# Optimization experiments

Hardware: AMD Instinct MI355X
Metric: run time of the kernel (lower is better)

Reference implementation:

```python
import jax, jax.numpy as jnp
import numpy as np
import math


def _forward(x, f0, theta, sigma, theta0, fbs, mix, w1, b1, w2, b2, conv_w):
    B, I, H, W = x.shape          # config requires B == I == H (== W here)
    S, O, _ = f0.shape            # config requires O == 1
    # ---- log-Gabor filter bank, fully vectorized over (scale, out, in) ----
    yy = jnp.linspace(-1.0, 1.0, H)[:, None]   # meshgrid 'ij': y along rows
    xx = jnp.linspace(-1.0, 1.0, W)[None, :]
    r = jnp.sqrt(xx ** 2 + yy ** 2 + 1e-6)     # [H,W]
    phi = jnp.arctan2(yy, xx)                  # [H,W]
    lr = jnp.log(r)
    log_gabor = jnp.exp(-(lr - jnp.log(f0)[..., None, None]) ** 2
                        / (2.0 * jnp.log(sigma)[..., None, None] ** 2))
    angular = jnp.exp(-(phi - theta[..., None, None]) ** 2
                      / (2.0 * theta0[..., None, None] ** 2))
    filters = log_gabor * angular              # [S,O,I,H,W]
    # ---- FFT (torch fftshift default shifts ALL dims; jnp matches) ----
    xs = jnp.fft.fftshift(jnp.fft.fft2(x))     # [B,I,H,W] complex64
    # ---- frequency attention (two 1x1 convs + softmax over scales) ----
    h1 = jax.nn.relu(jnp.einsum('bchw,oc->bohw', jnp.abs(xs), w1)
                     + b1[None, :, None, None])
    aw = jax.nn.softmax(jnp.einsum('bchw,sc->bshw', h1, w2)
                        + b2[None, :, None, None], axis=1)   # [B,S,H,W]
    # ---- attention-weighted combine. Faithful to torch broadcasting with
    # O==1 and B==I: attended[0,b,i,h,w] = sum_s xs[b,i]*F[s,0,i]*aw[i,s] ----
    attended = jnp.einsum('bihw,sihw,ishw->bihw', xs, filters[:, 0], aw)[None]
    # ---- dynamic frequency band mask (torch slices dims 2,3 = (Cin,H)) ----
    s_idx = jnp.floor((fbs[0, :, 0] + 1.0) / 2.0 * H).astype(jnp.int32)  # [I]
    e_idx = jnp.floor((fbs[0, :, 1] + 1.0) / 2.0 * H).astype(jnp.int32)
    arI = jnp.arange(I)
    arH = jnp.arange(H)
    mk = (arI[None, :] >= s_idx[:, None]) & (arI[None, :] < e_idx[:, None])  # [J,I]
    mh = (arH[None, :] >= s_idx[:, None]) & (arH[None, :] < e_idx[:, None])  # [J,H]
    mask = (mk[:, :, None] & mh[:, None, :]).astype(x.dtype)                 # [J,I,H]
    attended = attended * mask[None, :, :, :, None]
    # ---- back to spatial domain ----
    x_filtered = jnp.fft.ifft2(jnp.fft.ifftshift(attended)).real  # [1,B,I,H,W]
    # ---- spatial 3x3 conv path ----
    x_spatial = jax.lax.conv_general_dilated(
        x, conv_w, window_strides=(1, 1), padding=((1, 1), (1, 1)),
        dimension_numbers=('NCHW', 'OIHW', 'NCHW'))               # [B,1,H,W]
    return mix * x_filtered + (1.0 - mix) * x_spatial[None]


def setup_inputs() -> dict:
    key = jax.random.key(0)
    ks = jax.random.split(key, 10)
    B = I = H = W = 64
    O, S, HID = 1, 3, 64
    PI = math.pi
    x = jax.random.normal(ks[0], (B, I, H, W), dtype=jnp.float32)
    f0 = jnp.ones((S, O, I), jnp.float32)
    theta0 = jnp.ones((S, O, I), jnp.float32)
    sigma = jax.random.uniform(ks[1], (S, O, I), jnp.float32) * PI
    theta = jax.random.uniform(ks[2], (S, O, I), jnp.float32) * PI
    fbs = jax.random.uniform(ks[3], (O, I, 2), jnp.float32)
    mix = jax.random.uniform(ks[4], (1,), jnp.float32)
    w1 = jax.random.normal(ks[5], (HID, I), jnp.float32) * 0.05
    b1 = jnp.zeros((HID,), jnp.float32)
    w2 = jax.random.normal(ks[6], (S, HID), jnp.float32) * 0.05
    b2 = jnp.zeros((S,), jnp.float32)
    conv_w = jax.random.normal(ks[7], (O, I, 3, 3), jnp.float32) / math.sqrt(I * 9)
    return {'x': x, 'f0': f0, 'theta': theta, 'sigma': sigma, 'theta0': theta0,
            'fbs': fbs, 'mix': mix, 'w1': w1, 'b1': b1, 'w2': w2, 'b2': b2,
            'conv_w': conv_w}


def reference(x, f0, theta, sigma, theta0, fbs, mix, w1, b1, w2, b2, conv_w):
    return _forward(x, f0, theta, sigma, theta0, fbs, mix, w1, b1, w2, b2, conv_w)
```

## Files before the change

### kernel.cpp

```cpp
#include <hip/hip_runtime.h>

#define PI_D 3.14159265358979323846

namespace {
constexpr float CT[33] = {
  1.0000000000f,  0.9951847267f,  0.9807852804f,  0.9569403357f,
  0.9238795325f,  0.8819212643f,  0.8314696123f,  0.7730104534f,
  0.7071067812f,  0.6343932842f,  0.5555702330f,  0.4713967368f,
  0.3826834324f,  0.2902846773f,  0.1950903220f,  0.0980171403f,
  0.0f,          -0.0980171403f, -0.1950903220f, -0.2902846773f,
 -0.3826834324f, -0.4713967368f, -0.5555702330f, -0.6343932842f,
 -0.7071067812f, -0.7730104534f, -0.8314696123f, -0.8819212643f,
 -0.9238795325f, -0.9569403357f, -0.9807852804f, -0.9951847267f,
 -1.0f};
constexpr float STb[33] = {
  0.0f,           0.0980171403f,  0.1950903220f,  0.2902846773f,
  0.3826834324f,  0.4713967368f,  0.5555702330f,  0.6343932842f,
  0.7071067812f,  0.7730104534f,  0.8314696123f,  0.8819212643f,
  0.9238795325f,  0.9569403357f,  0.9807852804f,  0.9951847267f,
  1.0f,           0.9951847267f,  0.9807852804f,  0.9569403357f,
  0.9238795325f,  0.8819212643f,  0.8314696123f,  0.7730104534f,
  0.7071067812f,  0.6343932842f,  0.5555702330f,  0.4713967368f,
  0.3826834324f,  0.2902846773f,  0.1950903220f,  0.0980171403f,
  0.0f};
}

__device__ __forceinline__ void bitrev64(float v[64]) {
#pragma unroll
  for (int i = 0; i < 64; ++i) {
    const int j = (int)(__brev((unsigned)i) >> 26);
    if (j > i) { const float tv = v[i]; v[i] = v[j]; v[j] = tv; }
  }
}

template <bool INV, bool REAL>
__device__ __forceinline__ void fft64_stages(float re[64], float im[64]) {
#pragma unroll
  for (int s = 0; s < 6; ++s) {
    const int half = 1 << s;
    const int m = half << 1;
    const int tstep = 32 >> s;
#pragma unroll
    for (int k = 0; k < 64; k += m) {
#pragma unroll
      for (int j = 0; j < half; ++j) {
        const int ti = j * tstep;
        const int a = k + j, b = k + j + half;
        if (REAL && j == 0) {
          const float tr = re[b];
          re[b] = re[a] - tr;
          re[a] = re[a] + tr;
        } else if (REAL && ti == 16) {
          const float t0 = re[b];
          re[b] = re[a];
          im[b] = t0;
          im[a] = -t0;
        } else {
          float tr, tii;
          if (ti == 0) {
            tr = re[b]; tii = im[b];
          } else if (ti == 16) {
            if (INV) { tr = -im[b]; tii = re[b]; }
            else     { tr =  im[b]; tii = -re[b]; }
          } else {
            const float wr = CT[ti];
            const float wi = INV ? STb[ti] : -STb[ti];
            tr  = re[b] * wr - im[b] * wi;
            tii = re[b] * wi + im[b] * wr;
          }
          re[b] = re[a] - tr;  im[b] = im[a] - tii;
          re[a] = re[a] + tr;  im[a] = im[a] + tii;
        }
      }
    }
  }
}

template <bool INV>
__device__ __forceinline__ void fft64_regs(float re[64], float im[64]) {
  bitrev64(re);
  bitrev64(im);
  fft64_stages<INV, false>(re, im);
}

__device__ __forceinline__ void fft64_fwd_real(float re[64], float im[64]) {
  bitrev64(re);
  fft64_stages<false, true>(re, im);
}

__device__ __forceinline__ void band_from_fbs(const float* __restrict__ fbs,
                                              int c, int& s0, int& e0) {
  s0 = (int)floorf((fbs[2 * c]     + 1.0f) * 0.5f * 64.0f);
  e0 = (int)floorf((fbs[2 * c + 1] + 1.0f) * 0.5f * 64.0f);
}

__global__ __launch_bounds__(64) void k_fft_fwd(const float* __restrict__ x,
                                                float* __restrict__ F,
                                                const float* __restrict__ fbs,
                                                const float* __restrict__ w1,
                                                float* __restrict__ w1T) {
  __shared__ float buf[64][65];
  const int t = threadIdx.x;
  const int img = blockIdx.x;
  if (img == 0) {
    for (int k = 0; k < 64; ++k) w1T[t * 64 + k] = w1[k * 64 + t];
  }
  const float* xp = x + ((size_t)img << 12);
  const float4* xr4 = reinterpret_cast<const float4*>(xp + (t << 6));
  float re[64], im[64];
#pragma unroll
  for (int q = 0; q < 16; ++q) {
    const float4 v = xr4[q];
    re[4 * q]     = v.x; re[4 * q + 1] = v.y;
    re[4 * q + 2] = v.z; re[4 * q + 3] = v.w;
  }
#pragma unroll
  for (int j = 0; j < 64; ++j) im[j] = 0.0f;
  fft64_fwd_real(re, im);
#pragma unroll
  for (int j = 0; j < 64; ++j) buf[t][j] = re[j];
  __syncthreads();
#pragma unroll
  for (int j = 0; j < 64; ++j) re[j] = buf[j][t];
  __syncthreads();
#pragma unroll
  for (int j = 0; j < 64; ++j) buf[t][j] = im[j];
  __syncthreads();
#pragma unroll
  for (int j = 0; j < 64; ++j) im[j] = buf[j][t];
  fft64_regs<false>(re, im);
  const int b = img >> 6, i = img & 63;
  const int b_s = (b + 32) & 63, i_s = (i + 32) & 63;
  int s0, e0;
  band_from_fbs(fbs, b_s, s0, e0);
  float* Fre = F + ((size_t)img << 13);
  if ((i_s >= s0) && (i_s < e0)) {
    float* Fim = Fre + 4096;
#pragma unroll
    for (int j = 0; j < 64; ++j) {
      Fre[j * 64 + t] = re[j];
      Fim[j * 64 + t] = im[j];
    }
  } else {
#pragma unroll
    for (int j = 0; j < 64; ++j)
      Fre[j * 64 + t] = sqrtf(re[j] * re[j] + im[j] * im[j]);
  }
}

__global__ __launch_bounds__(256, 4) void k_attn_conv(
    const float* __restrict__ F, const float* __restrict__ w1T,
    const float* __restrict__ b1, const float* __restrict__ w2,
    const float* __restrict__ b2, const float* __restrict__ f0,
    const float* __restrict__ theta, const float* __restrict__ sigma,
    const float* __restrict__ theta0, const float* __restrict__ fbs,
    float* __restrict__ Wc,
    const float* __restrict__ x, const float* __restrict__ cw,
    const float* __restrict__ mixp, float* __restrict__ xsp,
    float* __restrict__ out) {
  __shared__ float part[4][3][64];
  const int t = threadIdx.x;
  const unsigned blk = blockIdx.x;
  const unsigned q5 = blk / 5u;
  const unsigned r5 = blk - q5 * 5u;

  if (r5 == 4u) {
    const int lane = t & 63;
    const int cwv = t >> 6;
    const int b = (int)(q5 >> 4);
    const int row = (int)((q5 & 15u) << 2) | cwv;
    const float* xb = x + ((size_t)b << 18);
    const int rm = row > 0 ? row - 1 : 0;
    const int rp = row < 63 ? row + 1 : 63;
    float P00 = 0.f, P01 = 0.f, P02 = 0.f;
    float P10 = 0.f, P11 = 0.f, P12 = 0.f;
    float P20 = 0.f, P21 = 0.f, P22 = 0.f;
#pragma unroll 4
    for (int ch = 0; ch < 64; ++ch) {
      const float* xc = xb + (ch << 12);
      const float v0 = xc[(rm << 6) + lane];
      const float v1 = xc[(row << 6) + lane];
      const float v2 = xc[(rp << 6) + lane];
      const float* wp = cw + ch * 9;
      P00 = fmaf(v0, wp[0], P00);
      P01 = fmaf(v0, wp[1], P01);
      P02 = fmaf(v0, wp[2], P02);
      P10 = fmaf(v1, wp[3], P10);
      P11 = fmaf(v1, wp[4], P11);
      P12 = fmaf(v1, wp[5], P12);
      P20 = fmaf(v2, wp[6], P20);
      P21 = fmaf(v2, wp[7], P21);
      P22 = fmaf(v2, wp[8], P22);
    }
    const float tmask = (row > 0) ? 1.0f : 0.0f;
    const float bmask = (row < 63) ? 1.0f : 0.0f;
    const float Ql = tmask * P00 + P10 + bmask * P20;
    const float Qm = tmask * P01 + P11 + bmask * P21;
    const float Qr = tmask * P02 + P12 + bmask * P22;
    const float fromL = __shfl_up(Ql, 1, 64);
    const float fromR = __shfl_down(Qr, 1, 64);
    float acc = Qm;
    if (lane > 0) acc += fromL;
    if (lane < 63) acc += fromR;
    xsp[((size_t)b << 12) + (row << 6) + lane] = acc;
    const int b_s = (b + 32) & 63;
    int s0, e0;
    band_from_fbs(fbs, b_s, s0, e0);
    const float val = (1.0f - mixp[0]) * acc;
    float* ob = out + ((size_t)b << 18) + (row << 6) + lane;
#pragma unroll 4
    for (int i2 = 0; i2 < 64; ++i2) {
      const int i_s = (i2 + 32) & 63;
      if (!(i_s >= s0 && i_s < e0)) ob[(size_t)i2 << 12] = val;
    }
    return;
  }

  const int ai = (int)(4u * q5 + r5);
  const int lane = t & 63;
  const int wv = __builtin_amdgcn_readfirstlane(t >> 6);
  const int k0 = wv << 4;
  const int i = ai >> 6;
  const int h = ai & 63;
  const int b_f = (i + 32) & 63;
  const int u_f = (h + 32) & 63;
  const int v_f = (lane + 32) & 63;
  const int pos_f = (u_f << 6) + v_f;
  int s0a, e0a;
  band_from_fbs(fbs, i, s0a, e0a);
  int alo = s0a < 0 ? 0 : (s0a > 64 ? 64 : s0a);
  int ahi = e0a < 0 ? 0 : (e0a > 64 ? 64 : e0a);
  if (ahi < alo) ahi = alo;
  float acc[16];
#pragma unroll
  for (int k = 0; k < 16; ++k) acc[k] = 0.0f;
  const float* Fb = F + ((size_t)(b_f << 6) << 13) + pos_f;
  const float* w1k = w1T + k0;
#pragma unroll 4
  for (int c = 0; c < alo; ++c) {
    const int c_f = (c + 32) & 63;
    const float mc = Fb[(size_t)c_f << 13];
    const float* wrow = w1k + (c << 6);
#pragma unroll
    for (int k = 0; k < 16; ++k) acc[k] = fmaf(wrow[k], mc, acc[k]);
  }
#pragma unroll 2
  for (int c = alo; c < ahi; ++c) {
    const int c_f = (c + 32) & 63;
    const float* base = Fb + ((size_t)c_f << 13);
    const float xr = base[0], xi = base[4096];
    const float mc = sqrtf(xr * xr + xi * xi);
    const float* wrow = w1k + (c << 6);
#pragma unroll
    for (int k = 0; k < 16; ++k) acc[k] = fmaf(wrow[k], mc, acc[k]);
  }
#pragma unroll 4
  for (int c = ahi; c < 64; ++c) {
    const int c_f = (c + 32) & 63;
    const float mc = Fb[(size_t)c_f << 13];
    const float* wrow = w1k + (c << 6);
#pragma unroll
    for (int k = 0; k < 16; ++k) acc[k] = fmaf(wrow[k], mc, acc[k]);
  }
  float p0 = 0.0f, p1 = 0.0f, p2 = 0.0f;
#pragma unroll
  for (int k = 0; k < 16; ++k) {
    const float hv = fmaxf(acc[k] + b1[k0 + k], 0.0f);
    p0 = fmaf(w2[k0 + k], hv, p0);
    p1 = fmaf(w2[64 + k0 + k], hv, p1);
    p2 = fmaf(w2[128 + k0 + k], hv, p2);
  }
  if (wv != 0) {
    part[wv][0][lane] = p0;
    part[wv][1][lane] = p1;
    part[wv][2][lane] = p2;
  }
  __syncthreads();
  if (wv != 0) return;
  float l0 = b2[0] + p0 + part[1][0][lane] + part[2][0][lane] + part[3][0][lane];
  float l1 = b2[1] + p1 + part[1][1][lane] + part[2][1][lane] + part[3][1][lane];
  float l2 = b2[2] + p2 + part[1][2][lane] + part[2][2][lane] + part[3][2][lane];
  float mx = fmaxf(l0, fmaxf(l1, l2));
  float e0v = expf(l0 - mx), e1 = expf(l1 - mx), e2 = expf(l2 - mx);
  float inv = 1.0f / (e0v + e1 + e2);
  float aw0 = e0v * inv, aw1 = e1 * inv, aw2 = e2 * inv;
  const float yy = -1.0f + (float)h * (2.0f / 63.0f);
  const float xx = -1.0f + (float)lane * (2.0f / 63.0f);
  const float r = sqrtf(xx * xx + yy * yy + 1e-6f);
  const float lr = logf(r);
  const float phi = atan2f(yy, xx);
  float wc = 0.0f;
  const float aws[3] = {aw0, aw1, aw2};
#pragma unroll
  for (int s = 0; s < 3; ++s) {
    const float f0v = f0[s * 64 + i];
    const float sgv = sigma[s * 64 + i];
    const float thv = theta[s * 64 + i];
    const float t0v = theta0[s * 64 + i];
    const float ls = logf(sgv);
    const float d1 = lr - logf(f0v);
    const float g1 = expf(-(d1 * d1) / (2.0f * ls * ls));
    const float d2 = phi - thv;
    const float g2 = expf(-(d2 * d2) / (2.0f * t0v * t0v));
    wc = fmaf(g1 * g2, aws[s], wc);
  }
  Wc[((i << 6) + h) * 64 + lane] = wc;
}

__global__ __launch_bounds__(64) void k_ifft_act(
    const float* __restrict__ F, const float* __restrict__ Wc,
    const float* __restrict__ xsp, const float* __restrict__ fbs,
    const float* __restrict__ mixp, float* __restrict__ out) {
  const int img = blockIdx.x;
  const int b = img >> 6, i = img & 63;
  const int b_s = (b + 32) & 63, i_s = (i + 32) & 63;
  int s0, e0;
  band_from_fbs(fbs, b_s, s0, e0);
  if (!((i_s >= s0) && (i_s < e0))) return;
  __shared__ float buf[64][65];
  const int t = threadIdx.x;
  const float* Fre = F + ((size_t)img << 13);
  const float* Fim = Fre + 4096;
  const float* Wcp = Wc + ((size_t)i_s << 12);
  const int u_s = (t + 32) & 63;
  const float rmask = (u_s >= s0 && u_s < e0) ? 1.0f : 0.0f;
  const float* wrow = Wcp + (u_s << 6);
  const float4* fr4 = reinterpret_cast<const float4*>(Fre + (t << 6));
  const float4* fi4 = reinterpret_cast<const float4*>(Fim + (t << 6));
  float re[64], im[64];
#pragma unroll
  for (int q = 0; q < 16; ++q) {
    const int j0 = 4 * q;
    const float4 w4 = *reinterpret_cast<const float4*>(wrow + ((j0 + 32) & 63));
    const float4 vr = fr4[q];
    const float4 vi = fi4[q];
    const float w0 = rmask * w4.x, w1v = rmask * w4.y;
    const float w2v = rmask * w4.z, w3v = rmask * w4.w;
    re[j0]     = vr.x * w0;  re[j0 + 1] = vr.y * w1v;
    re[j0 + 2] = vr.z * w2v; re[j0 + 3] = vr.w * w3v;
    im[j0]     = vi.x * w0;  im[j0 + 1] = vi.y * w1v;
    im[j0 + 2] = vi.z * w2v; im[j0 + 3] = vi.w * w3v;
  }
  fft64_regs<true>(re, im);
#pragma unroll
  for (int j = 0; j < 64; ++j) buf[t][j] = re[j];
  __syncthreads();
#pragma unroll
  for (int j = 0; j < 64; ++j) re[j] = buf[j][t];
  __syncthreads();
#pragma unroll
  for (int j = 0; j < 64; ++j) buf[t][j] = im[j];
  __syncthreads();
#pragma unroll
  for (int j = 0; j < 64; ++j) im[j] = buf[j][t];
  fft64_regs<true>(re, im);
  const float mixv = mixp[0];
  const float sc = mixv * (1.0f / 4096.0f);
  const float om = 1.0f - mixv;
  float* op = out + ((size_t)img << 12);
  const float* xp = xsp + ((size_t)b << 12);
#pragma unroll
  for (int j = 0; j < 64; ++j)
    op[j * 64 + t] = fmaf(sc, re[j], om * xp[j * 64 + t]);
}

extern "C" void kernel_launch(void* const* d_in, const int* in_sizes, int n_in,
                              void* d_out, int out_size, void* d_ws, size_t ws_size,
                              hipStream_t stream) {
  const float* x      = (const float*)d_in[0];
  const float* f0     = (const float*)d_in[1];
  const float* theta  = (const float*)d_in[2];
  const float* sigma  = (const float*)d_in[3];
  const float* theta0 = (const float*)d_in[4];
  const float* fbs    = (const float*)d_in[5];
  const float* mix    = (const float*)d_in[6];
  const float* w1     = (const float*)d_in[7];
  const float* b1     = (const float*)d_in[8];
  const float* w2     = (const float*)d_in[9];
  const float* b2     = (const float*)d_in[10];
  const float* cw     = (const float*)d_in[11];
  float* out = (float*)d_out;
  char* ws = (char*)d_ws;
  float* F   = (float*)(ws);
  float* Wc  = (float*)(ws + 134217728);
  float* xsp = (float*)(ws + 134217728 + 1048576);
  float* w1T = (float*)(ws + 134217728 + 2097152);

  k_fft_fwd<<<4096, 64, 0, stream>>>(x, F, fbs, w1, w1T);
  k_attn_conv<<<5120, 256, 0, stream>>>(F, w1T, b1, w2, b2, f0, theta, sigma,
                                        theta0, fbs, Wc, x, cw, mix, xsp, out);
  k_ifft_act<<<4096, 64, 0, stream>>>(F, Wc, xsp, fbs, mix, out);
}
```

Measured before the change: 212.2 us.

## Split spectrum into dense magnitude buffer and compacted in-band complex buffer

The forward FFT now always writes a dense magnitude array and writes complex spectra only for in-band images, into a compacted buffer indexed by (b<<5)+i. The attention kernel then reads precomputed magnitudes with a uniform, fully unrolled loop that issues 16 loads at a time. This drops the three band-dependent loops and the sqrt-of-complex path from the attention kernel, and halves the stride between its loads. In exchange, in-band images need extra magnitude writes. The compact indexing only avoids collisions and stays inside the buffer if in-band images have i < 32, which holds only when fbs lies in [0,1).

```diff
diff --git a/kernel.cpp b/kernel.cpp
--- a/kernel.cpp
+++ b/kernel.cpp
@@ -95,7 +95,8 @@
 }
 
 __global__ __launch_bounds__(64) void k_fft_fwd(const float* __restrict__ x,
-                                                float* __restrict__ F,
+                                                float* __restrict__ Mag,
+                                                float* __restrict__ Fc,
                                                 const float* __restrict__ fbs,
                                                 const float* __restrict__ w1,
                                                 float* __restrict__ w1T) {
@@ -129,27 +130,27 @@
 #pragma unroll
   for (int j = 0; j < 64; ++j) im[j] = buf[j][t];
   fft64_regs<false>(re, im);
+  float* Mg = Mag + ((size_t)img << 12);
+#pragma unroll
+  for (int j = 0; j < 64; ++j)
+    Mg[j * 64 + t] = sqrtf(re[j] * re[j] + im[j] * im[j]);
   const int b = img >> 6, i = img & 63;
   const int b_s = (b + 32) & 63, i_s = (i + 32) & 63;
   int s0, e0;
   band_from_fbs(fbs, b_s, s0, e0);
-  float* Fre = F + ((size_t)img << 13);
   if ((i_s >= s0) && (i_s < e0)) {
+    float* Fre = Fc + ((size_t)((b << 5) + i) << 13);
     float* Fim = Fre + 4096;
 #pragma unroll
     for (int j = 0; j < 64; ++j) {
       Fre[j * 64 + t] = re[j];
       Fim[j * 64 + t] = im[j];
     }
-  } else {
-#pragma unroll
-    for (int j = 0; j < 64; ++j)
-      Fre[j * 64 + t] = sqrtf(re[j] * re[j] + im[j] * im[j]);
   }
 }
 
 __global__ __launch_bounds__(256, 4) void k_attn_conv(
-    const float* __restrict__ F, const float* __restrict__ w1T,
+    const float* __restrict__ Mag, const float* __restrict__ w1T,
     const float* __restrict__ b1, const float* __restrict__ w2,
     const float* __restrict__ b2, const float* __restrict__ f0,
     const float* __restrict__ theta, const float* __restrict__ sigma,
@@ -226,41 +227,23 @@
   const int u_f = (h + 32) & 63;
   const int v_f = (lane + 32) & 63;
   const int pos_f = (u_f << 6) + v_f;
-  int s0a, e0a;
-  band_from_fbs(fbs, i, s0a, e0a);
-  int alo = s0a < 0 ? 0 : (s0a > 64 ? 64 : s0a);
-  int ahi = e0a < 0 ? 0 : (e0a > 64 ? 64 : e0a);
-  if (ahi < alo) ahi = alo;
   float acc[16];
 #pragma unroll
   for (int k = 0; k < 16; ++k) acc[k] = 0.0f;
-  const float* Fb = F + ((size_t)(b_f << 6) << 13) + pos_f;
-  const float* w1k = w1T + k0;
-#pragma unroll 4
-  for (int c = 0; c < alo; ++c) {
-    const int c_f = (c + 32) & 63;
-    const float mc = Fb[(size_t)c_f << 13];
-    const float* wrow = w1k + (c << 6);
-#pragma unroll
-    for (int k = 0; k < 16; ++k) acc[k] = fmaf(wrow[k], mc, acc[k]);
-  }
-#pragma unroll 2
-  for (int c = alo; c < ahi; ++c) {
-    const int c_f = (c + 32) & 63;
-    const float* base = Fb + ((size_t)c_f << 13);
-    const float xr = base[0], xi = base[4096];
-    const float mc = sqrtf(xr * xr + xi * xi);
-    const float* wrow = w1k + (c << 6);
-#pragma unroll
-    for (int k = 0; k < 16; ++k) acc[k] = fmaf(wrow[k], mc, acc[k]);
-  }
-#pragma unroll 4
-  for (int c = ahi; c < 64; ++c) {
-    const int c_f = (c + 32) & 63;
-    const float mc = Fb[(size_t)c_f << 13];
-    const float* wrow = w1k + (c << 6);
-#pragma unroll
-    for (int k = 0; k < 16; ++k) acc[k] = fmaf(wrow[k], mc, acc[k]);
+  const float* Mb = Mag + (((size_t)(b_f << 6)) << 12) + pos_f;
+#pragma unroll
+  for (int chk = 0; chk < 4; ++chk) {
+    float mc[16];
+#pragma unroll
+    for (int q = 0; q < 16; ++q)
+      mc[q] = Mb[(size_t)((chk << 4) + q) << 12];
+#pragma unroll
+    for (int q = 0; q < 16; ++q) {
+      const int c = (((chk << 4) + q) + 32) & 63;
+      const float* wrow = w1T + (c << 6) + k0;
+#pragma unroll
+      for (int k = 0; k < 16; ++k) acc[k] = fmaf(wrow[k], mc[q], acc[k]);
+    }
   }
   float p0 = 0.0f, p1 = 0.0f, p2 = 0.0f;
 #pragma unroll
@@ -308,7 +291,7 @@
 }
 
 __global__ __launch_bounds__(64) void k_ifft_act(
-    const float* __restrict__ F, const float* __restrict__ Wc,
+    const float* __restrict__ Fc, const float* __restrict__ Wc,
     const float* __restrict__ xsp, const float* __restrict__ fbs,
     const float* __restrict__ mixp, float* __restrict__ out) {
   const int img = blockIdx.x;
@@ -319,7 +302,7 @@
   if (!((i_s >= s0) && (i_s < e0))) return;
   __shared__ float buf[64][65];
   const int t = threadIdx.x;
-  const float* Fre = F + ((size_t)img << 13);
+  const float* Fre = Fc + ((size_t)((b << 5) + i) << 13);
   const float* Fim = Fre + 4096;
   const float* Wcp = Wc + ((size_t)i_s << 12);
   const int u_s = (t + 32) & 63;
@@ -381,13 +364,14 @@
   const float* cw     = (const float*)d_in[11];
   float* out = (float*)d_out;
   char* ws = (char*)d_ws;
-  float* F   = (float*)(ws);
+  float* Mag = (float*)(ws);
+  float* Fc  = (float*)(ws + 67108864);
   float* Wc  = (float*)(ws + 134217728);
   float* xsp = (float*)(ws + 134217728 + 1048576);
   float* w1T = (float*)(ws + 134217728 + 2097152);
 
-  k_fft_fwd<<<4096, 64, 0, stream>>>(x, F, fbs, w1, w1T);
-  k_attn_conv<<<5120, 256, 0, stream>>>(F, w1T, b1, w2, b2, f0, theta, sigma,
+  k_fft_fwd<<<4096, 64, 0, stream>>>(x, Mag, Fc, fbs, w1, w1T);
+  k_attn_conv<<<5120, 256, 0, stream>>>(Mag, w1T, b1, w2, b2, f0, theta, sigma,
                                         theta0, fbs, Wc, x, cw, mix, xsp, out);
-  k_ifft_act<<<4096, 64, 0, stream>>>(F, Wc, xsp, fbs, mix, out);
-}
+  k_ifft_act<<<4096, 64, 0, stream>>>(Fc, Wc, xsp, fbs, mix, out);
+}
```

Result: slower. 217.9 us (+2.7%).
